# Optimization experiments

Measured on AMD Instinct MI355X. Metric: run time of the kernel, lower is better.

The kernel has to match this reference:

```python
import jax, jax.numpy as jnp
import numpy as np

SHAPE0 = (256, 256)   # top pyramid level (h, w)
SIGMA = 3.0
EPS = 1e-3
BATCH = 128
N_CHAN = 3
N_LEVELS = 4
N_PIX = sum((SHAPE0[0] >> i) * (SHAPE0[1] >> i) for i in range(N_LEVELS))  # 87040


def _gauss_lum_kernel(sigma):
    # 2D Gaussian times RGB luminance weights -> HWIO kernel (kh, kw, 3, 1)
    s = int(np.ceil(2 * sigma))
    u = np.linspace(-s, s, 2 * s + 1)
    g = np.exp(-(u[:, None] ** 2 + u[None, :] ** 2) / (2 * sigma ** 2)) / (2 * np.pi * sigma ** 2)
    w = np.array([0.2989, 0.587, 0.114])
    k = (g[:, :, None, None] * w[None, None, :, None]).astype(np.float32)
    return jnp.asarray(k)


def _conv_same(x, k):
    # NHWC conv with zero 'SAME' padding; equivalent to the original
    # pad(s) + SAME conv + center crop (net effect is SAME with zero pad).
    return jax.lax.conv_general_dilated(
        x, k, window_strides=(1, 1), padding='SAME',
        dimension_numbers=('NHWC', 'HWIO', 'NHWC'))


def setup_inputs() -> dict:
    key = jax.random.key(0)
    x = jax.random.uniform(key, (BATCH, N_PIX, N_CHAN), dtype=jnp.float32)
    return {"x": x}


def reference(x):
    k = _gauss_lum_kernel(SIGMA)
    n_pix, nc = x.shape[1], x.shape[2]
    h, w = SHAPE0
    outs = []
    i = 0
    while i + h * w <= n_pix:  # static Python loop over pyramid levels
        xi = x[:, i:i + h * w, :].reshape(-1, h, w, nc)          # (B,h,w,3)
        lum = _conv_same(xi, k)                                   # (B,h,w,1)
        dens = _conv_same(jnp.ones((1, h, w, nc), x.dtype), k)    # (1,h,w,1), input-independent
        outs.append((xi / (lum / dens + EPS)).reshape(-1, h * w, nc))
        i += h * w
        h //= 2
        w //= 2
    return jnp.concatenate(outs, axis=1)  # packed pyramid (B, n_pix, 3)
```

## Files before the change

kernel.cpp:

```cpp
#include <hip/hip_runtime.h>


#define NPIX   87040
#define EPSV   1e-3f
#define WSUM   0.9999f
#define TW     64
#define TH     16
#define RAD    6
#define LW     80
#define LH     28
#define NG     (LH * 20)

__device__ __constant__ float G1[13] = {
    0.01799699f, 0.03315904f, 0.05467002f, 0.08065689f, 0.10648267f,
    0.12579441f, 0.13298076f, 0.12579441f, 0.10648267f, 0.08065689f,
    0.05467002f, 0.03315904f, 0.01799699f
};
__device__ __constant__ float PRE[14] = {
    0.00000000f, 0.01799699f, 0.05115603f, 0.10582605f, 0.18648294f,
    0.29296561f, 0.41876002f, 0.55174078f, 0.67753519f, 0.78401786f,
    0.86467475f, 0.91934477f, 0.95250381f, 0.97050080f
};

__global__ __launch_bounds__(256)
void mslln_kernel(const float* __restrict__ x, float* __restrict__ out) {
    __shared__ float s_lum[LH][LW];
    __shared__ float s_rc[LH][TW];
    __shared__ float s_scale[TH][TW];

    const int bid = blockIdx.x;
    const int t   = threadIdx.x;

    int img, tl, txlog, h, off;
    if (bid < 8192)       { img = bid >> 6;                 tl = bid & 63; txlog = 2; h = 256; off = 0;     }
    else if (bid < 10240) { int r = bid - 8192;  img = r >> 4; tl = r & 15; txlog = 1; h = 128; off = 65536; }
    else if (bid < 10752) { int r = bid - 10240; img = r >> 2; tl = r & 3;  txlog = 0; h = 64;  off = 81920; }
    else                  { int r = bid - 10752; img = r >> 1; tl = r & 1;  txlog = 0; h = 32;  off = 86016; }
    const int w   = h;
    const int tx0 = (tl & ((1 << txlog) - 1)) << 6;
    const int ty0 = (tl >> txlog) << 4;

    const float* __restrict__ xb = x   + (size_t)img * (NPIX * 3) + (size_t)off * 3;
    float*       __restrict__ ob = out + (size_t)img * (NPIX * 3) + (size_t)off * 3;

#pragma unroll
    for (int k = 0; k < 3; k++) {
        unsigned i = t + k * 256;
        if (i < NG) {
            int gr  = i / 20;
            int gc  = i - gr * 20;
            int gy  = ty0 + gr - RAD;
            int gx0 = tx0 + (gc << 2) - 8;
            float4 f0 = {0,0,0,0}, f1 = {0,0,0,0}, f2 = {0,0,0,0};
            if (gy >= 0 && gy < h) {
                if (gx0 >= 0 && gx0 + 3 < w) {
                    const float4* p = (const float4*)(xb + ((size_t)gy * w + gx0) * 3);
                    f0 = p[0]; f1 = p[1]; f2 = p[2];
                } else {
                    float v[12];
#pragma unroll
                    for (int c = 0; c < 12; c++) v[c] = 0.f;
#pragma unroll
                    for (int c = 0; c < 4; c++) {
                        int gx = gx0 + c;
                        if (gx >= 0 && gx < w) {
                            const float* s = xb + ((size_t)gy * w + gx) * 3;
                            v[3*c] = s[0]; v[3*c+1] = s[1]; v[3*c+2] = s[2];
                        }
                    }
                    f0 = make_float4(v[0], v[1], v[2],  v[3]);
                    f1 = make_float4(v[4], v[5], v[6],  v[7]);
                    f2 = make_float4(v[8], v[9], v[10], v[11]);
                }
            }
            float l0 = 0.2989f*f0.x + 0.587f*f0.y + 0.114f*f0.z;
            float l1 = 0.2989f*f0.w + 0.587f*f1.x + 0.114f*f1.y;
            float l2 = 0.2989f*f1.z + 0.587f*f1.w + 0.114f*f2.x;
            float l3 = 0.2989f*f2.y + 0.587f*f2.z + 0.114f*f2.w;
            *(float4*)&s_lum[gr][gc << 2] = make_float4(l0, l1, l2, l3);
        }
    }
    __syncthreads();

#pragma unroll
    for (int k = 0; k < 7; k++) {
        int i = t + k * 256;
        int r = i >> 6, c = i & 63;
        float s = 0.f;
#pragma unroll
        for (int j = 0; j < 13; j++) s += s_lum[r][c + 2 + j] * G1[j];
        s_rc[r][c] = s;
    }
    __syncthreads();

#pragma unroll
    for (int k = 0; k < 4; k++) {
        int i  = t + k * 256;
        int ly = i >> 6, lx = i & 63;
        if (tx0 + lx < w) {
            float s = 0.f;
#pragma unroll
            for (int j = 0; j < 13; j++) s += s_rc[ly + j][lx] * G1[j];
            int gy = ty0 + ly, gx = tx0 + lx;
            int ylo = min(RAD, gy), yhi = min(RAD, h - 1 - gy);
            int xlo = min(RAD, gx), xhi = min(RAD, w - 1 - gx);
            float Sy = PRE[RAD + yhi + 1] - PRE[RAD - ylo];
            float Sx = PRE[RAD + xhi + 1] - PRE[RAD - xlo];
            float dens = WSUM * Sy * Sx;
            s_scale[ly][lx] = 1.0f / (s / dens + EPSV);
        }
    }
    __syncthreads();

    {
        int gr  = t >> 4;
        int gc  = t & 15;
        int gx0 = tx0 + (gc << 2);
        if (gx0 < w) {
            int gy = ty0 + gr;
            const float4* p = (const float4*)(xb + ((size_t)gy * w + gx0) * 3);
            float4 f0 = p[0], f1 = p[1], f2 = p[2];
            float4 sc = *(const float4*)&s_scale[gr][gc << 2];
            f0.x *= sc.x; f0.y *= sc.x; f0.z *= sc.x; f0.w *= sc.y;
            f1.x *= sc.y; f1.y *= sc.y; f1.z *= sc.z; f1.w *= sc.z;
            f2.x *= sc.z; f2.y *= sc.w; f2.z *= sc.w; f2.w *= sc.w;
            float4* q = (float4*)(ob + ((size_t)gy * w + gx0) * 3);
            q[0] = f0; q[1] = f1; q[2] = f2;
        }
    }
}

extern "C" void kernel_launch(void* const* d_in, const int* in_sizes, int n_in,
                              void* d_out, int out_size, void* d_ws, size_t ws_size,
                              hipStream_t stream) {
    const float* x = (const float*)d_in[0];
    float* out = (float*)d_out;
    mslln_kernel<<<11008, 256, 0, stream>>>(x, out);
}
```

Before: 244.9 us.

## Double tile height, keep interior RGB in registers, fuse scale into output pass

Raises the tile height from 16 to 32 rows, so the 6-row vertical halo is amortised over more output rows and the grid is halved. Each thread loads its interior RGB pixels once into registers, reuses them for both the luminance and the final scaling, and skips the second global read of x. The vertical convolution now computes four outputs per thread and applies the scale directly, which removes the s_scale buffer and one barrier. Output writes use nontemporal stores. The costs are higher register pressure under the 6-waves occupancy hint and fewer blocks on the small levels.

Result: slower. 284.3 us (+16.1%).

```diff
diff --git a/kernel.cpp b/kernel.cpp
--- a/kernel.cpp
+++ b/kernel.cpp
@@ -1,15 +1,16 @@
 #include <hip/hip_runtime.h>
 
+
+typedef float f4 __attribute__((ext_vector_type(4)));
 
 #define NPIX   87040
 #define EPSV   1e-3f
 #define WSUM   0.9999f
 #define TW     64
-#define TH     16
+#define TH     32
 #define RAD    6
 #define LW     80
-#define LH     28
-#define NG     (LH * 20)
+#define LH     44
 
 __device__ __constant__ float G1[13] = {
     0.01799699f, 0.03315904f, 0.05467002f, 0.08065689f, 0.10648267f,
@@ -22,68 +23,94 @@
     0.86467475f, 0.91934477f, 0.95250381f, 0.97050080f
 };
 
-__global__ __launch_bounds__(256)
+__global__ __launch_bounds__(256, 6)
 void mslln_kernel(const float* __restrict__ x, float* __restrict__ out) {
     __shared__ float s_lum[LH][LW];
     __shared__ float s_rc[LH][TW];
-    __shared__ float s_scale[TH][TW];
 
     const int bid = blockIdx.x;
     const int t   = threadIdx.x;
 
     int img, tl, txlog, h, off;
-    if (bid < 8192)       { img = bid >> 6;                 tl = bid & 63; txlog = 2; h = 256; off = 0;     }
-    else if (bid < 10240) { int r = bid - 8192;  img = r >> 4; tl = r & 15; txlog = 1; h = 128; off = 65536; }
-    else if (bid < 10752) { int r = bid - 10240; img = r >> 2; tl = r & 3;  txlog = 0; h = 64;  off = 81920; }
-    else                  { int r = bid - 10752; img = r >> 1; tl = r & 1;  txlog = 0; h = 32;  off = 86016; }
+    if (bid < 4096)      { img = bid >> 5;               tl = bid & 31; txlog = 2; h = 256; off = 0;     }
+    else if (bid < 5120) { int r = bid - 4096; img = r >> 3; tl = r & 7; txlog = 1; h = 128; off = 65536; }
+    else if (bid < 5376) { int r = bid - 5120; img = r >> 1; tl = r & 1; txlog = 0; h = 64;  off = 81920; }
+    else                 { img = bid - 5376;   tl = 0;       txlog = 0; h = 32;  off = 86016; }
     const int w   = h;
     const int tx0 = (tl & ((1 << txlog) - 1)) << 6;
-    const int ty0 = (tl >> txlog) << 4;
+    const int ty0 = (tl >> txlog) << 5;
 
     const float* __restrict__ xb = x   + (size_t)img * (NPIX * 3) + (size_t)off * 3;
     float*       __restrict__ ob = out + (size_t)img * (NPIX * 3) + (size_t)off * 3;
 
+    const int ogr  = t >> 4;
+    const int ogc  = t & 15;
+    const int ogx0 = tx0 + (ogc << 2);
+    f4 rgb[2][3];
+
 #pragma unroll
-    for (int k = 0; k < 3; k++) {
-        unsigned i = t + k * 256;
-        if (i < NG) {
-            int gr  = i / 20;
-            int gc  = i - gr * 20;
-            int gy  = ty0 + gr - RAD;
-            int gx0 = tx0 + (gc << 2) - 8;
-            float4 f0 = {0,0,0,0}, f1 = {0,0,0,0}, f2 = {0,0,0,0};
-            if (gy >= 0 && gy < h) {
-                if (gx0 >= 0 && gx0 + 3 < w) {
-                    const float4* p = (const float4*)(xb + ((size_t)gy * w + gx0) * 3);
-                    f0 = p[0]; f1 = p[1]; f2 = p[2];
-                } else {
-                    float v[12];
+    for (int g = 0; g < 2; g++) {
+        int ly = ogr + (g << 4);
+        int gy = ty0 + ly;
+        f4 f0 = 0.f, f1 = 0.f, f2 = 0.f;
+        if (ogx0 < w) {
+            const f4* p = (const f4*)(xb + ((size_t)gy * w + ogx0) * 3);
+            f0 = p[0]; f1 = p[1]; f2 = p[2];
+        }
+        rgb[g][0] = f0; rgb[g][1] = f1; rgb[g][2] = f2;
+        f4 l;
+        l.x = 0.2989f*f0.x + 0.587f*f0.y + 0.114f*f0.z;
+        l.y = 0.2989f*f0.w + 0.587f*f1.x + 0.114f*f1.y;
+        l.z = 0.2989f*f1.z + 0.587f*f1.w + 0.114f*f2.x;
+        l.w = 0.2989f*f2.y + 0.587f*f2.z + 0.114f*f2.w;
+        *(f4*)&s_lum[ly + RAD][(ogc << 2) + 8] = l;
+    }
+
 #pragma unroll
-                    for (int c = 0; c < 12; c++) v[c] = 0.f;
+    for (int k = 0; k < 4; k++) {
+        unsigned i = (unsigned)t + k * 256u;
+        if (i < 880u) {
+            int gr = (int)(i / 20u);
+            int gc = (int)(i - (unsigned)gr * 20u);
+            bool interior = (gr >= RAD) && (gr < RAD + TH) && (gc >= 2) && (gc < 18);
+            if (!interior) {
+                int gy  = ty0 + gr - RAD;
+                int gx0 = tx0 + (gc << 2) - 8;
+                f4 f0 = 0.f, f1 = 0.f, f2 = 0.f;
+                if (gy >= 0 && gy < h) {
+                    if (gx0 >= 0 && gx0 + 3 < w) {
+                        const f4* p = (const f4*)(xb + ((size_t)gy * w + gx0) * 3);
+                        f0 = p[0]; f1 = p[1]; f2 = p[2];
+                    } else {
+                        float v[12];
 #pragma unroll
-                    for (int c = 0; c < 4; c++) {
-                        int gx = gx0 + c;
-                        if (gx >= 0 && gx < w) {
-                            const float* s = xb + ((size_t)gy * w + gx) * 3;
-                            v[3*c] = s[0]; v[3*c+1] = s[1]; v[3*c+2] = s[2];
+                        for (int c = 0; c < 12; c++) v[c] = 0.f;
+#pragma unroll
+                        for (int c = 0; c < 4; c++) {
+                            int gx = gx0 + c;
+                            if (gx >= 0 && gx < w) {
+                                const float* s = xb + ((size_t)gy * w + gx) * 3;
+                                v[3*c] = s[0]; v[3*c+1] = s[1]; v[3*c+2] = s[2];
+                            }
                         }
+                        f0 = (f4){v[0], v[1], v[2],  v[3]};
+                        f1 = (f4){v[4], v[5], v[6],  v[7]};
+                        f2 = (f4){v[8], v[9], v[10], v[11]};
                     }
-                    f0 = make_float4(v[0], v[1], v[2],  v[3]);
-                    f1 = make_float4(v[4], v[5], v[6],  v[7]);
-                    f2 = make_float4(v[8], v[9], v[10], v[11]);
                 }
+                f4 l;
+                l.x = 0.2989f*f0.x + 0.587f*f0.y + 0.114f*f0.z;
+                l.y = 0.2989f*f0.w + 0.587f*f1.x + 0.114f*f1.y;
+                l.z = 0.2989f*f1.z + 0.587f*f1.w + 0.114f*f2.x;
+                l.w = 0.2989f*f2.y + 0.587f*f2.z + 0.114f*f2.w;
+                *(f4*)&s_lum[gr][gc << 2] = l;
             }
-            float l0 = 0.2989f*f0.x + 0.587f*f0.y + 0.114f*f0.z;
-            float l1 = 0.2989f*f0.w + 0.587f*f1.x + 0.114f*f1.y;
-            float l2 = 0.2989f*f1.z + 0.587f*f1.w + 0.114f*f2.x;
-            float l3 = 0.2989f*f2.y + 0.587f*f2.z + 0.114f*f2.w;
-            *(float4*)&s_lum[gr][gc << 2] = make_float4(l0, l1, l2, l3);
         }
     }
     __syncthreads();
 
 #pragma unroll
-    for (int k = 0; k < 7; k++) {
+    for (int k = 0; k < 11; k++) {
         int i = t + k * 256;
         int r = i >> 6, c = i & 63;
         float s = 0.f;
@@ -94,39 +121,35 @@
     __syncthreads();
 
 #pragma unroll
-    for (int k = 0; k < 4; k++) {
-        int i  = t + k * 256;
-        int ly = i >> 6, lx = i & 63;
-        if (tx0 + lx < w) {
-            float s = 0.f;
+    for (int g = 0; g < 2; g++) {
+        int ly = ogr + (g << 4);
+        int gy = ty0 + ly;
+        if (ogx0 >= w) continue;
+        f4 acc = 0.f;
 #pragma unroll
-            for (int j = 0; j < 13; j++) s += s_rc[ly + j][lx] * G1[j];
-            int gy = ty0 + ly, gx = tx0 + lx;
-            int ylo = min(RAD, gy), yhi = min(RAD, h - 1 - gy);
+        for (int j = 0; j < 13; j++) {
+            f4 v = *(const f4*)&s_rc[ly + j][ogc << 2];
+            acc += v * G1[j];
+        }
+        int ylo = min(RAD, gy), yhi = min(RAD, h - 1 - gy);
+        float Sy = PRE[RAD + yhi + 1] - PRE[RAD - ylo];
+        f4 sc;
+#pragma unroll
+        for (int c = 0; c < 4; c++) {
+            int gx  = ogx0 + c;
             int xlo = min(RAD, gx), xhi = min(RAD, w - 1 - gx);
-            float Sy = PRE[RAD + yhi + 1] - PRE[RAD - ylo];
-            float Sx = PRE[RAD + xhi + 1] - PRE[RAD - xlo];
+            float Sx   = PRE[RAD + xhi + 1] - PRE[RAD - xlo];
             float dens = WSUM * Sy * Sx;
-            s_scale[ly][lx] = 1.0f / (s / dens + EPSV);
+            sc[c] = 1.0f / (acc[c] / dens + EPSV);
         }
-    }
-    __syncthreads();
-
-    {
-        int gr  = t >> 4;
-        int gc  = t & 15;
-        int gx0 = tx0 + (gc << 2);
-        if (gx0 < w) {
-            int gy = ty0 + gr;
-            const float4* p = (const float4*)(xb + ((size_t)gy * w + gx0) * 3);
-            float4 f0 = p[0], f1 = p[1], f2 = p[2];
-            float4 sc = *(const float4*)&s_scale[gr][gc << 2];
-            f0.x *= sc.x; f0.y *= sc.x; f0.z *= sc.x; f0.w *= sc.y;
-            f1.x *= sc.y; f1.y *= sc.y; f1.z *= sc.z; f1.w *= sc.z;
-            f2.x *= sc.z; f2.y *= sc.w; f2.z *= sc.w; f2.w *= sc.w;
-            float4* q = (float4*)(ob + ((size_t)gy * w + gx0) * 3);
-            q[0] = f0; q[1] = f1; q[2] = f2;
-        }
+        f4 o0 = rgb[g][0], o1 = rgb[g][1], o2 = rgb[g][2];
+        o0.x *= sc.x; o0.y *= sc.x; o0.z *= sc.x; o0.w *= sc.y;
+        o1.x *= sc.y; o1.y *= sc.y; o1.z *= sc.z; o1.w *= sc.z;
+        o2.x *= sc.z; o2.y *= sc.w; o2.z *= sc.w; o2.w *= sc.w;
+        f4* q = (f4*)(ob + ((size_t)gy * w + ogx0) * 3);
+        __builtin_nontemporal_store(o0, q);
+        __builtin_nontemporal_store(o1, q + 1);
+        __builtin_nontemporal_store(o2, q + 2);
     }
 }
 
@@ -135,5 +158,5 @@
                               hipStream_t stream) {
     const float* x = (const float*)d_in[0];
     float* out = (float*)d_out;
-    mslln_kernel<<<11008, 256, 0, stream>>>(x, out);
+    mslln_kernel<<<5504, 256, 0, stream>>>(x, out);
 }
```
